# Optimization experiments

Measured on AMD Instinct MI355X. Metric: run time of the kernel, lower is better.

The kernel has to match this reference:

```python
import jax, jax.numpy as jnp
import numpy as np

N_NODES = 100000
N_EDGES = 1600000
N_MOVES = 200000
D = 256          # in_channels
H = 512          # hidden_dim

def setup_inputs() -> dict:
    key = jax.random.key(0)
    ks = jax.random.split(key, 6)
    node_embeddings = jax.random.normal(ks[0], (N_NODES, D), dtype=jnp.float32)
    edge_index = jax.random.randint(ks[1], (2, N_EDGES), 0, N_NODES, dtype=jnp.int64)
    move_edge_idxs = jax.random.randint(ks[2], (N_MOVES,), 0, N_EDGES, dtype=jnp.int64)
    # torch Linear weights: [out, in], scaled like kaiming-uniform-ish
    W1 = jax.random.normal(ks[3], (H, 2 * D), dtype=jnp.float32) * (1.0 / np.sqrt(2 * D))
    b1 = jnp.zeros((H,), dtype=jnp.float32)
    W2 = jax.random.normal(ks[4], (H // 2, H), dtype=jnp.float32) * (1.0 / np.sqrt(H))
    b2 = jnp.zeros((H // 2,), dtype=jnp.float32)
    W3 = jax.random.normal(ks[5], (1, H // 2), dtype=jnp.float32) * (1.0 / np.sqrt(H // 2))
    b3 = jnp.zeros((1,), dtype=jnp.float32)
    return {"node_embeddings": node_embeddings, "edge_index": edge_index,
            "move_edge_idxs": move_edge_idxs, "W1": W1, "b1": b1,
            "W2": W2, "b2": b2, "W3": W3, "b3": b3}

def reference(node_embeddings, edge_index, move_edge_idxs, W1, b1, W2, b2, W3, b3):
    # candidate_moves = edge_index[:, move_edge_idxs].T -> [n_moves, 2]
    src = edge_index[0, move_edge_idxs]          # [n_moves]
    tgt = edge_index[1, move_edge_idxs]          # [n_moves]
    emb_src = node_embeddings[src]               # [n_moves, D]
    emb_tgt = node_embeddings[tgt]               # [n_moves, D]
    x = jnp.concatenate([emb_src, emb_tgt], axis=-1)   # [n_moves, 2D]
    # 3-layer MLP (dropout is identity in eval mode)
    h = jax.nn.relu(x @ W1.T + b1)               # [n_moves, H]
    h = jax.nn.relu(h @ W2.T + b2)               # [n_moves, H//2]
    logits = (h @ W3.T + b3).squeeze(-1)         # [n_moves]
    return logits
```

## Files before the change

### kernel.cpp

```cpp
#include <hip/hip_runtime.h>
#include <hip/hip_bf16.h>

typedef __attribute__((ext_vector_type(4))) float f32x4;
typedef __attribute__((ext_vector_type(8))) short bfrag;
typedef __attribute__((ext_vector_type(4))) float facc;
typedef __attribute__((ext_vector_type(8))) ushort u16x8;

#define N_MOVES 200000
#define N_EDGES 1600000
#define DEMB 256
#define KD 512
#define H1D 512
#define H2D 256
#define MT 64
#define NTHREADS 1024

__device__ __forceinline__ ushort f2b(float f) {
  union { float f; unsigned u; } x; x.f = f;
  unsigned r = (x.u + 0x7fffu + ((x.u >> 16) & 1u)) >> 16;
  return (ushort)r;
}
__device__ __forceinline__ float b2f(ushort h) {
  union { unsigned u; float f; } x; x.u = ((unsigned)h) << 16;
  return x.f;
}

__global__ void convert_w(const float* __restrict__ W1, const float* __restrict__ W2,
                          ushort* __restrict__ Wb) {
  int i = (blockIdx.x * 256 + threadIdx.x) * 4;
  const int n1 = H1D * KD;
  if (i < n1) {
    f32x4 v = *(const f32x4*)(W1 + i);
    ushort4 h = { f2b(v.x), f2b(v.y), f2b(v.z), f2b(v.w) };
    *(ushort4*)(Wb + i) = h;
  } else {
    int j = i - n1;
    f32x4 v = *(const f32x4*)(W2 + j);
    ushort4 h = { f2b(v.x), f2b(v.y), f2b(v.z), f2b(v.w) };
    *(ushort4*)(Wb + n1 + j) = h;
  }
}

__global__ void convert_emb(const float* __restrict__ E, ushort* __restrict__ Eb) {
  int i = (blockIdx.x * 256 + threadIdx.x) * 8;
  f32x4 a = *(const f32x4*)(E + i);
  f32x4 b = *(const f32x4*)(E + i + 4);
  u16x8 h = { f2b(a.x), f2b(a.y), f2b(a.z), f2b(a.w),
              f2b(b.x), f2b(b.y), f2b(b.z), f2b(b.w) };
  *(u16x8*)(Eb + i) = h;
}

template<int EMBBF>
__global__ __launch_bounds__(NTHREADS, 2)
void fused_mlp(const float* __restrict__ emb,
               const ushort* __restrict__ embb,
               const int* __restrict__ edge_index,
               const int* __restrict__ move_idx,
               const ushort* __restrict__ W1b,
               const float* __restrict__ b1,
               const ushort* __restrict__ W2b,
               const float* __restrict__ b2,
               const float* __restrict__ W3,
               const float* __restrict__ b3,
               float* __restrict__ out)
{
  __shared__ ushort bufA[MT][KD];
  __shared__ ushort bufB[MT][KD];
  __shared__ int   s_src[MT], s_tgt[MT];
  __shared__ float sW3[H2D];

  const int tid  = threadIdx.x;
  const int lane = tid & 63;
  const int wave = tid >> 6;
  const int m0   = blockIdx.x * MT;

  if (tid < MT) {
    int e = move_idx[m0 + tid];
    s_src[tid] = edge_index[e];
    s_tgt[tid] = edge_index[N_EDGES + e];
  }
  if (tid < H2D) sW3[tid] = W3[tid];
  __syncthreads();

  const int arow = lane & 15;
  const int akE  = (lane >> 4) << 3;
  const int akB  = (lane >> 4) << 4;

  const ushort* w1base = W1b + (size_t)(((wave << 5) + arow) * KD) + akE;
  bfrag b1a[2], b1b[2];
  #pragma unroll
  for (int ng = 0; ng < 2; ++ng) {
    b1a[ng] = *(const bfrag*)(w1base + (ng << 4) * KD);
    b1b[ng] = *(const bfrag*)(w1base + (ng << 4) * KD + 32);
  }
  float bias1[2];
  #pragma unroll
  for (int ng = 0; ng < 2; ++ng) bias1[ng] = b1[(wave << 5) + (ng << 4) + arow];

  if (EMBBF) {
    #pragma unroll
    for (int it = 0; it < (MT * 64) / NTHREADS; ++it) {
      int u   = tid + it * NTHREADS;
      int row = u >> 6;
      int c8  = u & 63;
      const ushort* sp = (c8 < 32) ? (embb + (size_t)s_src[row] * DEMB + (c8 << 3))
                                   : (embb + (size_t)s_tgt[row] * DEMB + ((c8 - 32) << 3));
      u16x8 v = *(const u16x8*)sp;
      int bo = (c8 << 4) ^ ((row & 7) << 4);
      *(u16x8*)((char*)(&bufA[row][0]) + bo) = v;
    }
  } else {
    #pragma unroll
    for (int it = 0; it < (MT * 128) / NTHREADS; ++it) {
      int u   = tid + it * NTHREADS;
      int row = u >> 7;
      int c4  = u & 127;
      const float* sp = (c4 < 64) ? (emb + (size_t)s_src[row] * DEMB + (c4 << 2))
                                  : (emb + (size_t)s_tgt[row] * DEMB + ((c4 - 64) << 2));
      f32x4 v = *(const f32x4*)sp;
      ushort4 h = { f2b(v.x), f2b(v.y), f2b(v.z), f2b(v.w) };
      int bo = (c4 << 3) ^ ((row & 7) << 4);
      *(ushort4*)((char*)(&bufA[row][0]) + bo) = h;
    }
  }
  __syncthreads();

  {
    facc acc[4][2] = {};
    bfrag a_c[4], a_n[4], b_n[2];
    #pragma unroll
    for (int mg = 0; mg < 4; ++mg) {
      int row = (mg << 4) + arow;
      int bo = akB ^ ((row & 7) << 4);
      a_c[mg] = *(const bfrag*)((const char*)(&bufA[row][0]) + bo);
    }
    #pragma unroll
    for (int kk = 0; kk < 16; ++kk) {
      if (kk < 15) {
        #pragma unroll
        for (int mg = 0; mg < 4; ++mg) {
          int row = (mg << 4) + arow;
          int bo = (((kk + 1) << 6) + akB) ^ ((row & 7) << 4);
          a_n[mg] = *(const bfrag*)((const char*)(&bufA[row][0]) + bo);
        }
      }
      if (kk < 14) {
        #pragma unroll
        for (int ng = 0; ng < 2; ++ng)
          b_n[ng] = *(const bfrag*)(w1base + (ng << 4) * KD + ((kk + 2) << 5));
      }
      #pragma unroll
      for (int mg = 0; mg < 4; ++mg)
        #pragma unroll
        for (int ng = 0; ng < 2; ++ng)
          acc[mg][ng] = __builtin_amdgcn_mfma_f32_16x16x32_bf16(a_c[mg], b1a[ng], acc[mg][ng], 0, 0, 0);
      #pragma unroll
      for (int mg = 0; mg < 4; ++mg) a_c[mg] = a_n[mg];
      #pragma unroll
      for (int ng = 0; ng < 2; ++ng) { b1a[ng] = b1b[ng]; b1b[ng] = b_n[ng]; }
    }

    const ushort* w2base = W2b + (size_t)(((wave << 4) + arow) * KD) + akE;
    bfrag b2a = *(const bfrag*)(w2base);
    bfrag b2b = *(const bfrag*)(w2base + 32);
    float bias2 = b2[(wave << 4) + arow];

    #pragma unroll
    for (int ng = 0; ng < 2; ++ng) {
      int col = (wave << 5) + (ng << 4) + arow;
      #pragma unroll
      for (int mg = 0; mg < 4; ++mg) {
        #pragma unroll
        for (int r = 0; r < 4; ++r) {
          int row = (mg << 4) + ((lane >> 4) << 2) + r;
          float v = fmaxf(acc[mg][ng][r] + bias1[ng], 0.f);
          int bo = (col << 1) ^ ((row & 7) << 4);
          *(ushort*)((char*)(&bufB[row][0]) + bo) = f2b(v);
        }
      }
    }
    __syncthreads();

    ushort (*H2s)[H2D] = (ushort(*)[H2D])bufA;
    {
      facc acc2[4] = {};
      bfrag a2c[4], a2n[4], b2n;
      #pragma unroll
      for (int mg = 0; mg < 4; ++mg) {
        int row = (mg << 4) + arow;
        int bo = akB ^ ((row & 7) << 4);
        a2c[mg] = *(const bfrag*)((const char*)(&bufB[row][0]) + bo);
      }
      #pragma unroll
      for (int kk = 0; kk < 16; ++kk) {
        if (kk < 15) {
          #pragma unroll
          for (int mg = 0; mg < 4; ++mg) {
            int row = (mg << 4) + arow;
            int bo = (((kk + 1) << 6) + akB) ^ ((row & 7) << 4);
            a2n[mg] = *(const bfrag*)((const char*)(&bufB[row][0]) + bo);
          }
        }
        if (kk < 14) b2n = *(const bfrag*)(w2base + ((kk + 2) << 5));
        #pragma unroll
        for (int mg = 0; mg < 4; ++mg)
          acc2[mg] = __builtin_amdgcn_mfma_f32_16x16x32_bf16(a2c[mg], b2a, acc2[mg], 0, 0, 0);
        #pragma unroll
        for (int mg = 0; mg < 4; ++mg) a2c[mg] = a2n[mg];
        b2a = b2b; b2b = b2n;
      }
      int col = (wave << 4) + arow;
      #pragma unroll
      for (int mg = 0; mg < 4; ++mg) {
        #pragma unroll
        for (int r = 0; r < 4; ++r) {
          int row = (mg << 4) + ((lane >> 4) << 2) + r;
          float v = fmaxf(acc2[mg][r] + bias2, 0.f);
          int bo = (col << 1) ^ ((row & 7) << 4);
          *(ushort*)((char*)(&H2s[row][0]) + bo) = f2b(v);
        }
      }
    }
  }
  __syncthreads();

  {
    ushort (*H2s)[H2D] = (ushort(*)[H2D])bufA;
    const float b3v = b3[0];
    int row = tid >> 4;
    int six = tid & 15;
    float sum = 0.f;
    #pragma unroll
    for (int j = 0; j < 2; ++j) {
      int kb = (six << 5) + (j << 4);
      int bo = kb ^ ((row & 7) << 4);
      bfrag hv = *(const bfrag*)((const char*)(&H2s[row][0]) + bo);
      int k0 = (six << 4) + (j << 3);
      #pragma unroll
      for (int e = 0; e < 8; ++e)
        sum += b2f((ushort)hv[e]) * sW3[k0 + e];
    }
    sum += __shfl_xor(sum, 1);
    sum += __shfl_xor(sum, 2);
    sum += __shfl_xor(sum, 4);
    sum += __shfl_xor(sum, 8);
    if (six == 0) out[m0 + row] = sum + b3v;
  }
}

extern "C" void kernel_launch(void* const* d_in, const int* in_sizes, int n_in,
                              void* d_out, int out_size, void* d_ws, size_t ws_size,
                              hipStream_t stream) {
  const float* emb        = (const float*)d_in[0];
  const int*   edge_index = (const int*)d_in[1];
  const int*   move_idx   = (const int*)d_in[2];
  const float* W1         = (const float*)d_in[3];
  const float* b1         = (const float*)d_in[4];
  const float* W2         = (const float*)d_in[5];
  const float* b2         = (const float*)d_in[6];
  const float* W3         = (const float*)d_in[7];
  const float* b3         = (const float*)d_in[8];
  float* out = (float*)d_out;

  ushort* Wb   = (ushort*)d_ws;
  ushort* Embb = Wb + (H1D * KD + H2D * KD);
  const size_t need = (size_t)(H1D * KD + H2D * KD + 100000 * DEMB) * 2;

  convert_w<<<384, 256, 0, stream>>>(W1, W2, Wb);

  if (ws_size >= need) {
    convert_emb<<<12500, 256, 0, stream>>>(emb, Embb);
    fused_mlp<1><<<N_MOVES / MT, NTHREADS, 0, stream>>>(
        emb, Embb, edge_index, move_idx,
        Wb, b1, Wb + H1D * KD, b2, W3, b3, out);
  } else {
    fused_mlp<0><<<N_MOVES / MT, NTHREADS, 0, stream>>>(
        emb, Embb, edge_index, move_idx,
        Wb, b1, Wb + H1D * KD, b2, W3, b3, out);
  }
}
```

Baseline: 512.2 us.

## Halve block size, widen per-wave tiles, and drop second LDS buffer

Moves from 1024 to 512 threads per block. Each wave now computes a 64x64 tile in layer 1 and 64x32 in layer 2, so each A fragment read from shared memory feeds more MFMAs. The second 64KB shared buffer is removed by reusing bufA for the hidden activations, behind an added barrier, which lowers LDS use per block so up to 4 blocks can be resident per CU. The gather now issues all global loads before the shared stores. The trade-off is more accumulator registers per thread, register pressure under launch_bounds 4, and the loss of A-fragment prefetch across k steps.

```diff
diff --git a/kernel.cpp b/kernel.cpp
--- a/kernel.cpp
+++ b/kernel.cpp
@@ -13,7 +13,7 @@
 #define H1D 512
 #define H2D 256
 #define MT 64
-#define NTHREADS 1024
+#define NTHREADS 512
 
 __device__ __forceinline__ ushort f2b(float f) {
   union { float f; unsigned u; } x; x.f = f;
@@ -51,7 +51,7 @@
 }
 
 template<int EMBBF>
-__global__ __launch_bounds__(NTHREADS, 2)
+__global__ __launch_bounds__(NTHREADS, 4)
 void fused_mlp(const float* __restrict__ emb,
                const ushort* __restrict__ embb,
                const int* __restrict__ edge_index,
@@ -65,7 +65,6 @@
                float* __restrict__ out)
 {
   __shared__ ushort bufA[MT][KD];
-  __shared__ ushort bufB[MT][KD];
   __shared__ int   s_src[MT], s_tgt[MT];
   __shared__ float sW3[H2D];
 
@@ -86,33 +85,38 @@
   const int akE  = (lane >> 4) << 3;
   const int akB  = (lane >> 4) << 4;
 
-  const ushort* w1base = W1b + (size_t)(((wave << 5) + arow) * KD) + akE;
-  bfrag b1a[2], b1b[2];
-  #pragma unroll
-  for (int ng = 0; ng < 2; ++ng) {
-    b1a[ng] = *(const bfrag*)(w1base + (ng << 4) * KD);
-    b1b[ng] = *(const bfrag*)(w1base + (ng << 4) * KD + 32);
-  }
-  float bias1[2];
-  #pragma unroll
-  for (int ng = 0; ng < 2; ++ng) bias1[ng] = b1[(wave << 5) + (ng << 4) + arow];
+  const ushort* w1base = W1b + (size_t)(((wave << 6) + arow) * KD) + akE;
+  bfrag bcur[4], bnxt[4];
+  #pragma unroll
+  for (int ng = 0; ng < 4; ++ng) {
+    bcur[ng] = *(const bfrag*)(w1base + (ng << 4) * KD);
+    bnxt[ng] = *(const bfrag*)(w1base + (ng << 4) * KD + 32);
+  }
+  float bias1[4];
+  #pragma unroll
+  for (int ng = 0; ng < 4; ++ng) bias1[ng] = b1[(wave << 6) + (ng << 4) + arow];
 
   if (EMBBF) {
-    #pragma unroll
-    for (int it = 0; it < (MT * 64) / NTHREADS; ++it) {
+    u16x8 gv[8];
+    #pragma unroll
+    for (int it = 0; it < 8; ++it) {
       int u   = tid + it * NTHREADS;
       int row = u >> 6;
       int c8  = u & 63;
       const ushort* sp = (c8 < 32) ? (embb + (size_t)s_src[row] * DEMB + (c8 << 3))
                                    : (embb + (size_t)s_tgt[row] * DEMB + ((c8 - 32) << 3));
-      u16x8 v = *(const u16x8*)sp;
-      int bo = (c8 << 4) ^ ((row & 7) << 4);
-      *(u16x8*)((char*)(&bufA[row][0]) + bo) = v;
+      gv[it] = *(const u16x8*)sp;
+    }
+    #pragma unroll
+    for (int it = 0; it < 8; ++it) {
+      int u   = tid + it * NTHREADS;
+      int row = u >> 6;
+      int c8  = u & 63;
+      int bo  = (c8 << 4) ^ ((row & 7) << 4);
+      *(u16x8*)((char*)(&bufA[row][0]) + bo) = gv[it];
     }
   } else {
-    #pragma unroll
-    for (int it = 0; it < (MT * 128) / NTHREADS; ++it) {
-      int u   = tid + it * NTHREADS;
+    for (int u = tid; u < MT * 128; u += NTHREADS) {
       int row = u >> 7;
       int c4  = u & 127;
       const float* sp = (c4 < 64) ? (emb + (size_t)s_src[row] * DEMB + (c4 << 2))
@@ -125,117 +129,112 @@
   }
   __syncthreads();
 
+  facc acc[4][4] = {};
+  #pragma unroll
+  for (int kk = 0; kk < 16; ++kk) {
+    bfrag a[4];
+    #pragma unroll
+    for (int mg = 0; mg < 4; ++mg) {
+      int row = (mg << 4) + arow;
+      int bo = ((kk << 6) + akB) ^ ((row & 7) << 4);
+      a[mg] = *(const bfrag*)((const char*)(&bufA[row][0]) + bo);
+    }
+    bfrag bn[4];
+    if (kk < 14) {
+      #pragma unroll
+      for (int ng = 0; ng < 4; ++ng)
+        bn[ng] = *(const bfrag*)(w1base + (ng << 4) * KD + ((kk + 2) << 5));
+    }
+    #pragma unroll
+    for (int mg = 0; mg < 4; ++mg)
+      #pragma unroll
+      for (int ng = 0; ng < 4; ++ng)
+        acc[mg][ng] = __builtin_amdgcn_mfma_f32_16x16x32_bf16(a[mg], bcur[ng], acc[mg][ng], 0, 0, 0);
+    #pragma unroll
+    for (int ng = 0; ng < 4; ++ng) { bcur[ng] = bnxt[ng]; bnxt[ng] = bn[ng]; }
+  }
+
+  const ushort* w2base = W2b + (size_t)(((wave << 5) + arow) * KD) + akE;
+  bfrag ccur[2], cnxt[2];
+  ccur[0] = *(const bfrag*)(w2base);
+  ccur[1] = *(const bfrag*)(w2base + (KD << 4));
+  cnxt[0] = *(const bfrag*)(w2base + 32);
+  cnxt[1] = *(const bfrag*)(w2base + (KD << 4) + 32);
+  float bias2[2];
+  #pragma unroll
+  for (int ng = 0; ng < 2; ++ng) bias2[ng] = b2[(wave << 5) + (ng << 4) + arow];
+
+  __syncthreads();
+
+  #pragma unroll
+  for (int ng = 0; ng < 4; ++ng) {
+    int col = (wave << 6) + (ng << 4) + arow;
+    #pragma unroll
+    for (int mg = 0; mg < 4; ++mg) {
+      #pragma unroll
+      for (int r = 0; r < 4; ++r) {
+        int row = (mg << 4) + ((lane >> 4) << 2) + r;
+        float v = fmaxf(acc[mg][ng][r] + bias1[ng], 0.f);
+        int bo = (col << 1) ^ ((row & 7) << 4);
+        *(ushort*)((char*)(&bufA[row][0]) + bo) = f2b(v);
+      }
+    }
+  }
+  __syncthreads();
+
+  facc acc2[4][2] = {};
+  #pragma unroll
+  for (int kk = 0; kk < 16; ++kk) {
+    bfrag a[4];
+    #pragma unroll
+    for (int mg = 0; mg < 4; ++mg) {
+      int row = (mg << 4) + arow;
+      int bo = ((kk << 6) + akB) ^ ((row & 7) << 4);
+      a[mg] = *(const bfrag*)((const char*)(&bufA[row][0]) + bo);
+    }
+    bfrag cn[2];
+    if (kk < 14) {
+      cn[0] = *(const bfrag*)(w2base + ((kk + 2) << 5));
+      cn[1] = *(const bfrag*)(w2base + (KD << 4) + ((kk + 2) << 5));
+    }
+    #pragma unroll
+    for (int mg = 0; mg < 4; ++mg)
+      #pragma unroll
+      for (int ng = 0; ng < 2; ++ng)
+        acc2[mg][ng] = __builtin_amdgcn_mfma_f32_16x16x32_bf16(a[mg], ccur[ng], acc2[mg][ng], 0, 0, 0);
+    #pragma unroll
+    for (int ng = 0; ng < 2; ++ng) { ccur[ng] = cnxt[ng]; cnxt[ng] = cn[ng]; }
+  }
+  __syncthreads();
+
+  ushort (*H2s)[H2D] = (ushort(*)[H2D])bufA;
+  #pragma unroll
+  for (int ng = 0; ng < 2; ++ng) {
+    int col = (wave << 5) + (ng << 4) + arow;
+    #pragma unroll
+    for (int mg = 0; mg < 4; ++mg) {
+      #pragma unroll
+      for (int r = 0; r < 4; ++r) {
+        int row = (mg << 4) + ((lane >> 4) << 2) + r;
+        float v = fmaxf(acc2[mg][ng][r] + bias2[ng], 0.f);
+        int bo = (col << 1) ^ ((row & 7) << 4);
+        *(ushort*)((char*)(&H2s[row][0]) + bo) = f2b(v);
+      }
+    }
+  }
+  __syncthreads();
+
   {
-    facc acc[4][2] = {};
-    bfrag a_c[4], a_n[4], b_n[2];
-    #pragma unroll
-    for (int mg = 0; mg < 4; ++mg) {
-      int row = (mg << 4) + arow;
-      int bo = akB ^ ((row & 7) << 4);
-      a_c[mg] = *(const bfrag*)((const char*)(&bufA[row][0]) + bo);
-    }
-    #pragma unroll
-    for (int kk = 0; kk < 16; ++kk) {
-      if (kk < 15) {
-        #pragma unroll
-        for (int mg = 0; mg < 4; ++mg) {
-          int row = (mg << 4) + arow;
-          int bo = (((kk + 1) << 6) + akB) ^ ((row & 7) << 4);
-          a_n[mg] = *(const bfrag*)((const char*)(&bufA[row][0]) + bo);
-        }
-      }
-      if (kk < 14) {
-        #pragma unroll
-        for (int ng = 0; ng < 2; ++ng)
-          b_n[ng] = *(const bfrag*)(w1base + (ng << 4) * KD + ((kk + 2) << 5));
-      }
-      #pragma unroll
-      for (int mg = 0; mg < 4; ++mg)
-        #pragma unroll
-        for (int ng = 0; ng < 2; ++ng)
-          acc[mg][ng] = __builtin_amdgcn_mfma_f32_16x16x32_bf16(a_c[mg], b1a[ng], acc[mg][ng], 0, 0, 0);
-      #pragma unroll
-      for (int mg = 0; mg < 4; ++mg) a_c[mg] = a_n[mg];
-      #pragma unroll
-      for (int ng = 0; ng < 2; ++ng) { b1a[ng] = b1b[ng]; b1b[ng] = b_n[ng]; }
-    }
-
-    const ushort* w2base = W2b + (size_t)(((wave << 4) + arow) * KD) + akE;
-    bfrag b2a = *(const bfrag*)(w2base);
-    bfrag b2b = *(const bfrag*)(w2base + 32);
-    float bias2 = b2[(wave << 4) + arow];
-
-    #pragma unroll
-    for (int ng = 0; ng < 2; ++ng) {
-      int col = (wave << 5) + (ng << 4) + arow;
-      #pragma unroll
-      for (int mg = 0; mg < 4; ++mg) {
-        #pragma unroll
-        for (int r = 0; r < 4; ++r) {
-          int row = (mg << 4) + ((lane >> 4) << 2) + r;
-          float v = fmaxf(acc[mg][ng][r] + bias1[ng], 0.f);
-          int bo = (col << 1) ^ ((row & 7) << 4);
-          *(ushort*)((char*)(&bufB[row][0]) + bo) = f2b(v);
-        }
-      }
-    }
-    __syncthreads();
-
-    ushort (*H2s)[H2D] = (ushort(*)[H2D])bufA;
-    {
-      facc acc2[4] = {};
-      bfrag a2c[4], a2n[4], b2n;
-      #pragma unroll
-      for (int mg = 0; mg < 4; ++mg) {
-        int row = (mg << 4) + arow;
-        int bo = akB ^ ((row & 7) << 4);
-        a2c[mg] = *(const bfrag*)((const char*)(&bufB[row][0]) + bo);
-      }
-      #pragma unroll
-      for (int kk = 0; kk < 16; ++kk) {
-        if (kk < 15) {
-          #pragma unroll
-          for (int mg = 0; mg < 4; ++mg) {
-            int row = (mg << 4) + arow;
-            int bo = (((kk + 1) << 6) + akB) ^ ((row & 7) << 4);
-            a2n[mg] = *(const bfrag*)((const char*)(&bufB[row][0]) + bo);
-          }
-        }
-        if (kk < 14) b2n = *(const bfrag*)(w2base + ((kk + 2) << 5));
-        #pragma unroll
-        for (int mg = 0; mg < 4; ++mg)
-          acc2[mg] = __builtin_amdgcn_mfma_f32_16x16x32_bf16(a2c[mg], b2a, acc2[mg], 0, 0, 0);
-        #pragma unroll
-        for (int mg = 0; mg < 4; ++mg) a2c[mg] = a2n[mg];
-        b2a = b2b; b2b = b2n;
-      }
-      int col = (wave << 4) + arow;
-      #pragma unroll
-      for (int mg = 0; mg < 4; ++mg) {
-        #pragma unroll
-        for (int r = 0; r < 4; ++r) {
-          int row = (mg << 4) + ((lane >> 4) << 2) + r;
-          float v = fmaxf(acc2[mg][r] + bias2, 0.f);
-          int bo = (col << 1) ^ ((row & 7) << 4);
-          *(ushort*)((char*)(&H2s[row][0]) + bo) = f2b(v);
-        }
-      }
-    }
-  }
-  __syncthreads();
-
-  {
-    ushort (*H2s)[H2D] = (ushort(*)[H2D])bufA;
     const float b3v = b3[0];
-    int row = tid >> 4;
-    int six = tid & 15;
+    int row = tid >> 3;
+    int oct = tid & 7;
     float sum = 0.f;
     #pragma unroll
-    for (int j = 0; j < 2; ++j) {
-      int kb = (six << 5) + (j << 4);
+    for (int j = 0; j < 4; ++j) {
+      int kb = (oct << 6) + (j << 4);
       int bo = kb ^ ((row & 7) << 4);
       bfrag hv = *(const bfrag*)((const char*)(&H2s[row][0]) + bo);
-      int k0 = (six << 4) + (j << 3);
+      int k0 = (oct << 5) + (j << 3);
       #pragma unroll
       for (int e = 0; e < 8; ++e)
         sum += b2f((ushort)hv[e]) * sW3[k0 + e];
@@ -243,8 +242,7 @@
     sum += __shfl_xor(sum, 1);
     sum += __shfl_xor(sum, 2);
     sum += __shfl_xor(sum, 4);
-    sum += __shfl_xor(sum, 8);
-    if (six == 0) out[m0 + row] = sum + b3v;
+    if (oct == 0) out[m0 + row] = sum + b3v;
   }
 }
 
```

Result: slower. 784.4 us (+53.2%).
